# Kernel optimization log

Measured on AMD Instinct MI355X. Metric: run time of the kernel, lower is better.

Reference implementation:

```python
import jax, jax.numpy as jnp
import numpy as np


def setup_inputs() -> dict:
    key = jax.random.key(0)
    k1, k2, k3, k4 = jax.random.split(key, 4)
    B, N, F_in, F_out = 8, 2048, 256, 256
    inp = jax.random.normal(k1, (B, N, F_in), dtype=jnp.float32)
    adj = jax.random.uniform(k2, (B, N, N), dtype=jnp.float32)
    stdv = 1.0 / np.sqrt(F_out)
    weight = jax.random.uniform(k3, (F_in, F_out), dtype=jnp.float32, minval=-stdv, maxval=stdv)
    bias = jax.random.uniform(k4, (F_out,), dtype=jnp.float32, minval=-stdv, maxval=stdv)
    return {"input": inp, "adj": adj, "weight": weight, "bias": bias}


def reference(input, adj, weight, bias):
    # d = (sum over dim 1 of adj) ** -0.5, matching torch adj.sum(dim=1)
    d = adj.sum(axis=1) ** -0.5  # [B, N]
    # D @ A @ D with diagonal D -> row/col broadcast scaling (same math)
    adj_norm = d[:, :, None] * adj * d[:, None, :]  # [B, N, N]
    support = jnp.einsum('bnf,fo->bno', input, weight)  # [B, N, F_out]
    output = jnp.einsum('bnm,bmo->bno', adj_norm, support) + bias
    return output
```

## Files before the change

kernel.cpp:

```cpp
#include <hip/hip_runtime.h>

#define BATCH 8
#define NDIM 2048
#define FDIM 256
#define CH 32

typedef float f32x4 __attribute__((ext_vector_type(4)));
typedef short bf16x8 __attribute__((ext_vector_type(8)));
typedef short bf16x4 __attribute__((ext_vector_type(4)));

__device__ __forceinline__ short f2bf(float f) {
  union { float f; unsigned u; } v{f};
  return (short)((v.u + 0x7FFFu + ((v.u >> 16) & 1u)) >> 16);
}

__device__ __forceinline__ void gload_lds16(const void* g, void* l) {
  __builtin_amdgcn_global_load_lds(
      (const __attribute__((address_space(1))) void*)g,
      (__attribute__((address_space(3))) void*)l, 16, 0, 0);
}

__global__ __launch_bounds__(256) void k_colsum(const float* __restrict__ adj,
                                                float* __restrict__ part,
                                                short* __restrict__ abf) {
  int bid = blockIdx.x;
  int cb = bid & 1;
  int ch = (bid >> 1) & (CH - 1);
  int b = bid >> 6;
  int col = cb * 1024 + threadIdx.x * 4;
  size_t base = (size_t)b * NDIM * NDIM + (size_t)(ch * 64) * NDIM + col;
  const float* p = adj + base;
  short* q = abf + base;
  f32x4 acc = {0.f, 0.f, 0.f, 0.f};
#pragma unroll 8
  for (int i = 0; i < 64; ++i) {
    f32x4 v = *(const f32x4*)(p + (size_t)i * NDIM);
    acc += v;
    bf16x4 pk;
#pragma unroll
    for (int j = 0; j < 4; ++j) pk[j] = f2bf(v[j]);
    *(bf16x4*)(q + (size_t)i * NDIM) = pk;
  }
  *(f32x4*)(part + (size_t)(b * CH + ch) * NDIM + col) = acc;
}

__global__ __launch_bounds__(256) void k_small(const float* __restrict__ part,
                                               float* __restrict__ dnorm,
                                               const float* __restrict__ w,
                                               short* __restrict__ wt) {
  int t = threadIdx.x;
  if (blockIdx.x < 64) {
    int idx = blockIdx.x * 256 + t;
    int b = idx >> 11, j = idx & (NDIM - 1);
    float s = 0.f;
#pragma unroll
    for (int c = 0; c < CH; ++c) s += part[(size_t)(b * CH + c) * NDIM + j];
    dnorm[idx] = rsqrtf(s);
  } else {
    __shared__ float tile[64][65];
    int bb = blockIdx.x - 64;
    int bx = bb & 3, by = bb >> 2;
    int f0 = by * 64, o0 = bx * 64;
    int c4 = 4 * (t & 15);
#pragma unroll
    for (int q = 0; q < 4; ++q) {
      int r = (t >> 4) + 16 * q;
      f32x4 v = *(const f32x4*)(w + (size_t)(f0 + r) * FDIM + o0 + c4);
#pragma unroll
      for (int i = 0; i < 4; ++i) tile[r][c4 + i] = v[i];
    }
    __syncthreads();
#pragma unroll
    for (int q = 0; q < 4; ++q) {
      int r = (t >> 4) + 16 * q;
      bf16x4 pk;
#pragma unroll
      for (int i = 0; i < 4; ++i) pk[i] = f2bf(tile[c4 + i][r]);
      *(bf16x4*)(wt + (size_t)(o0 + r) * FDIM + f0 + c4) = pk;
    }
  }
}

__global__ __launch_bounds__(256) void k_support(const float* __restrict__ in,
                                                 const short* __restrict__ wt,
                                                 const float* __restrict__ dnorm,
                                                 short* __restrict__ st) {
  __shared__ short Al[64 * 32];
  __shared__ short Bl[256 * 32];
  int t = threadIdx.x, lane = t & 63, w = t >> 6;
  int b = blockIdx.x >> 5;
  int m0 = (blockIdx.x & 31) * 64;
  const float* inb = in + ((size_t)b * NDIM + m0) * FDIM;

  f32x4 acc[4][4];
#pragma unroll
  for (int m = 0; m < 4; ++m)
#pragma unroll
    for (int n = 0; n < 4; ++n) acc[m][n] = {0.f, 0.f, 0.f, 0.f};

  int ar = t >> 2, ac = t & 3;
  for (int it = 0; it < 8; ++it) {
    int k0 = it * 32;
    {
      f32x4 v0 = *(const f32x4*)(inb + (size_t)ar * FDIM + k0 + 8 * ac);
      f32x4 v1 = *(const f32x4*)(inb + (size_t)ar * FDIM + k0 + 8 * ac + 4);
      bf16x8 p;
#pragma unroll
      for (int i = 0; i < 4; ++i) { p[i] = f2bf(v0[i]); p[4 + i] = f2bf(v1[i]); }
      *(bf16x8*)&Al[ar * 32 + 8 * ac] = p;
    }
#pragma unroll
    for (int i = 0; i < 4; ++i) {
      int ss = i * 256 + t;
      int o = ss >> 2, c = ss & 3;
      gload_lds16(wt + (size_t)o * FDIM + k0 + 8 * c, &Bl[ss * 8]);
    }
    __syncthreads();
    bf16x8 af[4], bf[4];
#pragma unroll
    for (int m = 0; m < 4; ++m)
      af[m] = *(const bf16x8*)&Al[(16 * m + (lane & 15)) * 32 + (lane >> 4) * 8];
#pragma unroll
    for (int n = 0; n < 4; ++n)
      bf[n] = *(const bf16x8*)&Bl[(64 * w + 16 * n + (lane & 15)) * 32 + (lane >> 4) * 8];
#pragma unroll
    for (int m = 0; m < 4; ++m)
#pragma unroll
      for (int n = 0; n < 4; ++n)
        acc[m][n] = __builtin_amdgcn_mfma_f32_16x16x32_bf16(af[m], bf[n], acc[m][n], 0, 0, 0);
    __syncthreads();
  }
#pragma unroll
  for (int m = 0; m < 4; ++m) {
    int row = m0 + 16 * m + ((lane >> 4) << 2);
    float dm[4];
#pragma unroll
    for (int j = 0; j < 4; ++j) dm[j] = dnorm[b * NDIM + row + j];
#pragma unroll
    for (int n = 0; n < 4; ++n) {
      int col = 64 * w + 16 * n + (lane & 15);
      bf16x4 pk;
#pragma unroll
      for (int j = 0; j < 4; ++j) pk[j] = f2bf(acc[m][n][j] * dm[j]);
      *(bf16x4*)(st + ((size_t)(b * FDIM + col)) * NDIM + row) = pk;
    }
  }
}

__global__ __launch_bounds__(512) void k_main(const short* __restrict__ abf,
                                              const short* __restrict__ st,
                                              const float* __restrict__ dnorm,
                                              const float* __restrict__ bias,
                                              float* __restrict__ out) {
  __shared__ short Al[3][64 * 64];
  __shared__ short Bl[3][256 * 64];
  int t = threadIdx.x, lane = t & 63, w = t >> 6;
  int wm = w & 1, wn = w >> 1;
  int b = blockIdx.x & 7;
  int n0 = (blockIdx.x >> 3) * 64;
  const short* ab = abf + ((size_t)b * NDIM + n0) * NDIM;
  const short* stb = st + (size_t)b * FDIM * NDIM;

  int arow = t >> 3;
  int schk = (t & 7) ^ (arow & 7);
  const short* asrc = ab + (size_t)arow * NDIM + 8 * schk;
  const short* bsrc = stb + (size_t)arow * NDIM + 8 * schk;

  f32x4 acc[2][4];
#pragma unroll
  for (int m = 0; m < 2; ++m)
#pragma unroll
    for (int n = 0; n < 4; ++n) acc[m][n] = {0.f, 0.f, 0.f, 0.f};

  int lr = lane & 15, kg = lane >> 4, sw = lane & 7;

  auto stage = [&](int k, int bp) {
    int kc = k > 31 ? 31 : k;
    size_t ko = (size_t)kc * 64;
    gload_lds16(asrc + ko, &Al[bp][t * 8]);
#pragma unroll
    for (int i = 0; i < 4; ++i)
      gload_lds16(bsrc + (size_t)(i * 64) * NDIM + ko, &Bl[bp][(i * 512 + t) * 8]);
  };

  auto body = [&](int it, int bc, int bp) {
    stage(it + 2, bp);
    asm volatile("s_waitcnt vmcnt(10)" ::: "memory");
    __builtin_amdgcn_s_barrier();
    asm volatile("" ::: "memory");
    __builtin_amdgcn_sched_barrier(0);
#pragma unroll
    for (int h = 0; h < 2; ++h) {
      int kc = ((h * 4 + kg) ^ sw) * 8;
      bf16x8 af0 = *(const bf16x8*)&Al[bc][(wm * 32 + lr) * 64 + kc];
      bf16x8 af1 = *(const bf16x8*)&Al[bc][(wm * 32 + 16 + lr) * 64 + kc];
      bf16x8 bv0 = *(const bf16x8*)&Bl[bc][(wn * 64 + lr) * 64 + kc];
      bf16x8 bv1 = *(const bf16x8*)&Bl[bc][(wn * 64 + 16 + lr) * 64 + kc];
      bf16x8 bv2 = *(const bf16x8*)&Bl[bc][(wn * 64 + 32 + lr) * 64 + kc];
      bf16x8 bv3 = *(const bf16x8*)&Bl[bc][(wn * 64 + 48 + lr) * 64 + kc];
      acc[0][0] = __builtin_amdgcn_mfma_f32_16x16x32_bf16(af0, bv0, acc[0][0], 0, 0, 0);
      acc[0][1] = __builtin_amdgcn_mfma_f32_16x16x32_bf16(af0, bv1, acc[0][1], 0, 0, 0);
      acc[0][2] = __builtin_amdgcn_mfma_f32_16x16x32_bf16(af0, bv2, acc[0][2], 0, 0, 0);
      acc[0][3] = __builtin_amdgcn_mfma_f32_16x16x32_bf16(af0, bv3, acc[0][3], 0, 0, 0);
      acc[1][0] = __builtin_amdgcn_mfma_f32_16x16x32_bf16(af1, bv0, acc[1][0], 0, 0, 0);
      acc[1][1] = __builtin_amdgcn_mfma_f32_16x16x32_bf16(af1, bv1, acc[1][1], 0, 0, 0);
      acc[1][2] = __builtin_amdgcn_mfma_f32_16x16x32_bf16(af1, bv2, acc[1][2], 0, 0, 0);
      acc[1][3] = __builtin_amdgcn_mfma_f32_16x16x32_bf16(af1, bv3, acc[1][3], 0, 0, 0);
    }
    asm volatile("s_waitcnt lgkmcnt(0)" ::: "memory");
    __builtin_amdgcn_s_barrier();
    asm volatile("" ::: "memory");
  };

  stage(0, 0);
  stage(1, 1);

  for (int itb = 0; itb < 30; itb += 3) {
    body(itb + 0, 0, 2);
    body(itb + 1, 1, 0);
    body(itb + 2, 2, 1);
  }
  body(30, 0, 2);
  body(31, 1, 0);

#pragma unroll
  for (int mf = 0; mf < 2; ++mf) {
    int row = n0 + wm * 32 + mf * 16 + kg * 4;
    f32x4 dr = *(const f32x4*)&dnorm[b * NDIM + row];
#pragma unroll
    for (int nf = 0; nf < 4; ++nf) {
      int col = wn * 64 + nf * 16 + lr;
      float bv = bias[col];
      float* op = out + ((size_t)b * NDIM + row) * FDIM + col;
#pragma unroll
      for (int j = 0; j < 4; ++j) op[(size_t)j * FDIM] = dr[j] * acc[mf][nf][j] + bv;
    }
  }
}

extern "C" void kernel_launch(void* const* d_in, const int* in_sizes, int n_in,
                              void* d_out, int out_size, void* d_ws, size_t ws_size,
                              hipStream_t stream) {
  (void)in_sizes; (void)n_in; (void)out_size; (void)ws_size;
  const float* input = (const float*)d_in[0];
  const float* adj = (const float*)d_in[1];
  const float* weight = (const float*)d_in[2];
  const float* bias = (const float*)d_in[3];
  float* out = (float*)d_out;

  char* ws = (char*)d_ws;
  short* st = (short*)ws;
  float* dnorm = (float*)(ws + 8ull * 1024 * 1024);
  float* part = (float*)(ws + 8ull * 1024 * 1024 + 65536);
  short* wt = (short*)(ws + 8ull * 1024 * 1024 + 65536 + 2ull * 1024 * 1024);
  short* abf = (short*)(ws + 16ull * 1024 * 1024);

  k_colsum<<<dim3(BATCH * CH * 2), dim3(256), 0, stream>>>(adj, part, abf);
  k_small<<<dim3(80), dim3(256), 0, stream>>>(part, dnorm, weight, wt);
  k_support<<<dim3(BATCH * (NDIM / 64)), dim3(256), 0, stream>>>(input, wt, dnorm, st);
  k_main<<<dim3(BATCH * (NDIM / 64)), dim3(512), 0, stream>>>(abf, st, dnorm, bias, out);
}
```

Before: 79.92 us.

## Convert adjacency to bf16 inside main GEMM instead of materializing bf16 copy

The column-sum kernel no longer writes a bf16 copy of the adjacency matrix. The main GEMM kernel now streams fp32 adjacency tiles into LDS with a swizzled layout and converts them to bf16 in registers before the MFMAs. This removes a 64MB write and the intermediate buffer, and the second fp32 read of adj may partly hit in cache. In exchange, main-loop global reads of A double, LDS use grows, and conversion ALU work is added to the inner loop.

Result: slower. 81.84 us (+2.4%).

```diff
diff --git a/kernel.cpp b/kernel.cpp
--- a/kernel.cpp
+++ b/kernel.cpp
@@ -21,26 +21,16 @@
 }
 
 __global__ __launch_bounds__(256) void k_colsum(const float* __restrict__ adj,
-                                                float* __restrict__ part,
-                                                short* __restrict__ abf) {
+                                                float* __restrict__ part) {
   int bid = blockIdx.x;
   int cb = bid & 1;
   int ch = (bid >> 1) & (CH - 1);
   int b = bid >> 6;
   int col = cb * 1024 + threadIdx.x * 4;
-  size_t base = (size_t)b * NDIM * NDIM + (size_t)(ch * 64) * NDIM + col;
-  const float* p = adj + base;
-  short* q = abf + base;
+  const float* p = adj + (size_t)b * NDIM * NDIM + (size_t)(ch * 64) * NDIM + col;
   f32x4 acc = {0.f, 0.f, 0.f, 0.f};
 #pragma unroll 8
-  for (int i = 0; i < 64; ++i) {
-    f32x4 v = *(const f32x4*)(p + (size_t)i * NDIM);
-    acc += v;
-    bf16x4 pk;
-#pragma unroll
-    for (int j = 0; j < 4; ++j) pk[j] = f2bf(v[j]);
-    *(bf16x4*)(q + (size_t)i * NDIM) = pk;
-  }
+  for (int i = 0; i < 64; ++i) acc += *(const f32x4*)(p + (size_t)i * NDIM);
   *(f32x4*)(part + (size_t)(b * CH + ch) * NDIM + col) = acc;
 }
 
@@ -147,23 +137,27 @@
   }
 }
 
-__global__ __launch_bounds__(512) void k_main(const short* __restrict__ abf,
+__global__ __launch_bounds__(512) void k_main(const float* __restrict__ adj,
                                               const short* __restrict__ st,
                                               const float* __restrict__ dnorm,
                                               const float* __restrict__ bias,
                                               float* __restrict__ out) {
-  __shared__ short Al[3][64 * 64];
+  __shared__ float Alf[3][64 * 64];
   __shared__ short Bl[3][256 * 64];
   int t = threadIdx.x, lane = t & 63, w = t >> 6;
   int wm = w & 1, wn = w >> 1;
   int b = blockIdx.x & 7;
   int n0 = (blockIdx.x >> 3) * 64;
-  const short* ab = abf + ((size_t)b * NDIM + n0) * NDIM;
+  const float* ab = adj + ((size_t)b * NDIM + n0) * NDIM;
   const short* stb = st + (size_t)b * FDIM * NDIM;
 
+  int s0 = t, s1 = 512 + t;
+  int r0 = s0 >> 4, c0 = (s0 & 15) ^ ((r0 & 7) << 1);
+  int r1 = s1 >> 4, c1 = (s1 & 15) ^ ((r1 & 7) << 1);
+  const float* a0s = ab + (size_t)r0 * NDIM + c0 * 4;
+  const float* a1s = ab + (size_t)r1 * NDIM + c1 * 4;
   int arow = t >> 3;
   int schk = (t & 7) ^ (arow & 7);
-  const short* asrc = ab + (size_t)arow * NDIM + 8 * schk;
   const short* bsrc = stb + (size_t)arow * NDIM + 8 * schk;
 
   f32x4 acc[2][4];
@@ -172,12 +166,13 @@
 #pragma unroll
     for (int n = 0; n < 4; ++n) acc[m][n] = {0.f, 0.f, 0.f, 0.f};
 
-  int lr = lane & 15, kg = lane >> 4, sw = lane & 7;
+  int lr = lane & 15, kg = lane >> 4, sw = lane & 7, sw2 = (lane & 7) << 1;
 
   auto stage = [&](int k, int bp) {
     int kc = k > 31 ? 31 : k;
     size_t ko = (size_t)kc * 64;
-    gload_lds16(asrc + ko, &Al[bp][t * 8]);
+    gload_lds16(a0s + ko, &Alf[bp][s0 * 4]);
+    gload_lds16(a1s + ko, &Alf[bp][s1 * 4]);
 #pragma unroll
     for (int i = 0; i < 4; ++i)
       gload_lds16(bsrc + (size_t)(i * 64) * NDIM + ko, &Bl[bp][(i * 512 + t) * 8]);
@@ -185,27 +180,35 @@
 
   auto body = [&](int it, int bc, int bp) {
     stage(it + 2, bp);
-    asm volatile("s_waitcnt vmcnt(10)" ::: "memory");
+    asm volatile("s_waitcnt vmcnt(12)" ::: "memory");
     __builtin_amdgcn_s_barrier();
     asm volatile("" ::: "memory");
     __builtin_amdgcn_sched_barrier(0);
 #pragma unroll
     for (int h = 0; h < 2; ++h) {
-      int kc = ((h * 4 + kg) ^ sw) * 8;
-      bf16x8 af0 = *(const bf16x8*)&Al[bc][(wm * 32 + lr) * 64 + kc];
-      bf16x8 af1 = *(const bf16x8*)&Al[bc][(wm * 32 + 16 + lr) * 64 + kc];
+      int gk = h * 4 + kg;
+      bf16x8 af[2];
+#pragma unroll
+      for (int mf = 0; mf < 2; ++mf) {
+        const float* ap = &Alf[bc][(wm * 32 + mf * 16 + lr) * 64 + (((2 * gk) ^ sw2) * 4)];
+        f32x4 lo = *(const f32x4*)ap;
+        f32x4 hi = *(const f32x4*)(ap + 4);
+#pragma unroll
+        for (int j = 0; j < 4; ++j) { af[mf][j] = f2bf(lo[j]); af[mf][4 + j] = f2bf(hi[j]); }
+      }
+      int kc = (gk ^ sw) * 8;
       bf16x8 bv0 = *(const bf16x8*)&Bl[bc][(wn * 64 + lr) * 64 + kc];
       bf16x8 bv1 = *(const bf16x8*)&Bl[bc][(wn * 64 + 16 + lr) * 64 + kc];
       bf16x8 bv2 = *(const bf16x8*)&Bl[bc][(wn * 64 + 32 + lr) * 64 + kc];
       bf16x8 bv3 = *(const bf16x8*)&Bl[bc][(wn * 64 + 48 + lr) * 64 + kc];
-      acc[0][0] = __builtin_amdgcn_mfma_f32_16x16x32_bf16(af0, bv0, acc[0][0], 0, 0, 0);
-      acc[0][1] = __builtin_amdgcn_mfma_f32_16x16x32_bf16(af0, bv1, acc[0][1], 0, 0, 0);
-      acc[0][2] = __builtin_amdgcn_mfma_f32_16x16x32_bf16(af0, bv2, acc[0][2], 0, 0, 0);
-      acc[0][3] = __builtin_amdgcn_mfma_f32_16x16x32_bf16(af0, bv3, acc[0][3], 0, 0, 0);
-      acc[1][0] = __builtin_amdgcn_mfma_f32_16x16x32_bf16(af1, bv0, acc[1][0], 0, 0, 0);
-      acc[1][1] = __builtin_amdgcn_mfma_f32_16x16x32_bf16(af1, bv1, acc[1][1], 0, 0, 0);
-      acc[1][2] = __builtin_amdgcn_mfma_f32_16x16x32_bf16(af1, bv2, acc[1][2], 0, 0, 0);
-      acc[1][3] = __builtin_amdgcn_mfma_f32_16x16x32_bf16(af1, bv3, acc[1][3], 0, 0, 0);
+      acc[0][0] = __builtin_amdgcn_mfma_f32_16x16x32_bf16(af[0], bv0, acc[0][0], 0, 0, 0);
+      acc[0][1] = __builtin_amdgcn_mfma_f32_16x16x32_bf16(af[0], bv1, acc[0][1], 0, 0, 0);
+      acc[0][2] = __builtin_amdgcn_mfma_f32_16x16x32_bf16(af[0], bv2, acc[0][2], 0, 0, 0);
+      acc[0][3] = __builtin_amdgcn_mfma_f32_16x16x32_bf16(af[0], bv3, acc[0][3], 0, 0, 0);
+      acc[1][0] = __builtin_amdgcn_mfma_f32_16x16x32_bf16(af[1], bv0, acc[1][0], 0, 0, 0);
+      acc[1][1] = __builtin_amdgcn_mfma_f32_16x16x32_bf16(af[1], bv1, acc[1][1], 0, 0, 0);
+      acc[1][2] = __builtin_amdgcn_mfma_f32_16x16x32_bf16(af[1], bv2, acc[1][2], 0, 0, 0);
+      acc[1][3] = __builtin_amdgcn_mfma_f32_16x16x32_bf16(af[1], bv3, acc[1][3], 0, 0, 0);
     }
     asm volatile("s_waitcnt lgkmcnt(0)" ::: "memory");
     __builtin_amdgcn_s_barrier();
@@ -253,10 +256,9 @@
   float* dnorm = (float*)(ws + 8ull * 1024 * 1024);
   float* part = (float*)(ws + 8ull * 1024 * 1024 + 65536);
   short* wt = (short*)(ws + 8ull * 1024 * 1024 + 65536 + 2ull * 1024 * 1024);
-  short* abf = (short*)(ws + 16ull * 1024 * 1024);
-
-  k_colsum<<<dim3(BATCH * CH * 2), dim3(256), 0, stream>>>(adj, part, abf);
+
+  k_colsum<<<dim3(BATCH * CH * 2), dim3(256), 0, stream>>>(adj, part);
   k_small<<<dim3(80), dim3(256), 0, stream>>>(part, dnorm, weight, wt);
   k_support<<<dim3(BATCH * (NDIM / 64)), dim3(256), 0, stream>>>(input, wt, dnorm, st);
-  k_main<<<dim3(BATCH * (NDIM / 64)), dim3(512), 0, stream>>>(abf, st, dnorm, bias, out);
-}
+  k_main<<<dim3(BATCH * (NDIM / 64)), dim3(512), 0, stream>>>(adj, st, dnorm, bias, out);
+}
```
